# Kernel tuning notes

Measured on AMD Instinct MI355X. Metric: run time of the kernel, lower is better.

Reference implementation:

```python
import jax, jax.numpy as jnp
import numpy as np

B, S, D, H = 2, 2048, 1024, 16
HEAD_DIM = D // H  # 64


def setup_inputs() -> dict:
    key = jax.random.key(0)
    ks = jax.random.split(key, 7)
    x = jax.random.normal(ks[0], (B, S, D), dtype=jnp.float32)
    W_q = jax.random.normal(ks[1], (D, D), dtype=jnp.float32) * 0.02
    W_k = jax.random.normal(ks[2], (D, D), dtype=jnp.float32) * 0.02
    W_v = jax.random.normal(ks[3], (D, D), dtype=jnp.float32) * 0.02
    W_o = jax.random.normal(ks[4], (D, D), dtype=jnp.float32) * 0.02 / np.sqrt(2 * 12)
    b_o = jnp.zeros((D,), dtype=jnp.float32)
    # Ragged prefix attention_mask: per-row valid lengths in [S/2, S];
    # row 0 forced to full length so max_valid_len == S statically (jit-safe).
    lengths = jax.random.randint(ks[5], (B,), S // 2, S + 1)
    lengths = lengths.at[0].set(S)
    attention_mask = (jnp.arange(S)[None, :] < lengths[:, None]).astype(jnp.float32)
    return {"x": x, "attention_mask": attention_mask, "W_q": W_q, "W_k": W_k,
            "W_v": W_v, "W_o": W_o, "b_o": b_o}


def reference(x, attention_mask, W_q, W_k, W_v, W_o, b_o):
    b, s, d = x.shape
    h, hd = H, HEAD_DIM
    # QKV projections (no bias, qkv_bias=False)
    q = (x @ W_q.T).reshape(b, s, h, hd).transpose(0, 2, 1, 3)  # [b,h,s,hd]
    # Masking keys/values at invalid (padded) positions; for prefix masks this
    # is exactly the module's per-batch packing loop (max_valid_len == s).
    m = attention_mask[:, None, :, None]  # [b,1,s,1]
    k = ((x @ W_k.T).reshape(b, s, h, hd).transpose(0, 2, 1, 3)) * m
    v = ((x @ W_v.T).reshape(b, s, h, hd).transpose(0, 2, 1, 3)) * m
    # Naive causal attention, same op order as the torch module:
    # mask with -inf first, then scale by 1/sqrt(head_dim), then softmax.
    causal = jnp.triu(jnp.ones((s, s), dtype=bool), 1)  # True above diagonal
    scores = jnp.einsum('bhqd,bhkd->bhqk', q, k)
    scores = jnp.where(causal[None, None], -jnp.inf, scores)
    att = jax.nn.softmax(scores / jnp.sqrt(jnp.float32(hd)), axis=-1)
    ctx = jnp.einsum('bhqk,bhkd->bhqd', att, v)  # [b,h,s,hd]
    ctx = ctx.transpose(0, 2, 1, 3).reshape(b, s, d)
    # Output projection (dropout is inference no-op)
    return ctx @ W_o.T + b_o
```

## Files before the change

### kernel.cpp

```cpp
#include <hip/hip_runtime.h>

#define B_  2
#define S_  2048
#define D_  1024
#define H_  16
#define HD_ 64
#define N3_ 3072
#define M_  4096

typedef _Float16 f16;
typedef _Float16 f16x2 __attribute__((ext_vector_type(2)));
typedef _Float16 f16x4 __attribute__((ext_vector_type(4)));
typedef _Float16 f16x8 __attribute__((ext_vector_type(8)));
typedef float    f32x4 __attribute__((ext_vector_type(4)));

__device__ __forceinline__ void async16(const f16* g, f16* l) {
  __builtin_amdgcn_global_load_lds(
      (const __attribute__((address_space(1))) unsigned int*)g,
      (__attribute__((address_space(3))) unsigned int*)l, 16, 0, 0);
}

__device__ __forceinline__ f16x2 pkrtz(float a, float b) {
  return __builtin_bit_cast(f16x2, __builtin_amdgcn_cvt_pkrtz(a, b));
}

__global__ __launch_bounds__(256)
void cvt_all(const float* __restrict__ x,
             const float* __restrict__ Wq, const float* __restrict__ Wk,
             const float* __restrict__ Wv, const float* __restrict__ Wo,
             f16* __restrict__ xb, f16* __restrict__ wdst, float qscale) {
  const int i = blockIdx.x * 256 + threadIdx.x;
  const int XN4 = M_ * D_ / 4;
  const int WN4 = D_ * D_ / 4;
  const float* src;
  f16* dst;
  float scale = 1.0f;
  int j;
  if (i < XN4) {
    src = x; dst = xb; j = i;
  } else {
    int k = i - XN4;
    int m = k >> 18;
    j = k & (WN4 - 1);
    src = (m == 0) ? Wq : (m == 1) ? Wk : (m == 2) ? Wv : Wo;
    if (m == 0) scale = qscale;
    dst = wdst + (size_t)m * D_ * D_;
  }
  float4 v = ((const float4*)src)[j];
  f16x4 o = { (f16)(v.x * scale), (f16)(v.y * scale),
              (f16)(v.z * scale), (f16)(v.w * scale) };
  ((f16x4*)dst)[j] = o;
}

__global__ __launch_bounds__(256)
void gemm_qkv(const f16* __restrict__ A, const f16* __restrict__ Bw,
              f16* __restrict__ Cq, f16* __restrict__ vtout,
              const float* __restrict__ mask) {
  __shared__ f16 As[128 * 64];
  __shared__ f16 Bs[128 * 64];

  const int tid  = threadIdx.x;
  const int lane = tid & 63;
  const int w    = tid >> 6;
  const int lcol = lane & 15;
  const int quad = lane >> 4;
  const int lx   = lcol & 7;
  const int wave_m = w >> 1, wave_n = w & 1;

  const int m0 = blockIdx.y * 128;
  const int n0 = blockIdx.x * 128;

  const int rr  = lane >> 3;
  const int gch = (lane & 7) ^ rr;

  const f16* gA[4];
  const f16* gB[4];
  f16* lA[4];
  f16* lB[4];
#pragma unroll
  for (int i = 0; i < 4; i++) {
    int seg = i * 4 + w;
    int row = seg * 8 + rr;
    gA[i] = A  + (size_t)(m0 + row) * D_ + gch * 8;
    gB[i] = Bw + (size_t)(n0 + row) * D_ + gch * 8;
    lA[i] = As + seg * 512;
    lB[i] = Bs + seg * 512;
  }

  int offA[4], offB[4];
#pragma unroll
  for (int i = 0; i < 4; i++) {
    offA[i] = (wave_m * 64 + i * 16 + lcol) * 64;
    offB[i] = (wave_n * 64 + i * 16 + lcol) * 64;
  }

  const f32x4 zero = {0.f, 0.f, 0.f, 0.f};
  f32x4 acc[4][4];
#pragma unroll
  for (int i = 0; i < 4; i++)
#pragma unroll
    for (int j = 0; j < 4; j++) acc[i][j] = zero;

  for (int k0 = 0; k0 < D_; k0 += 64) {
    __syncthreads();
#pragma unroll
    for (int i = 0; i < 4; i++) async16(gA[i] + k0, lA[i]);
#pragma unroll
    for (int i = 0; i < 4; i++) async16(gB[i] + k0, lB[i]);
    __syncthreads();

#pragma unroll
    for (int ks = 0; ks < 2; ks++) {
      const int co = ((quad + 4 * ks) ^ lx) * 8;
      f16x8 af[4], bf[4];
#pragma unroll
      for (int i = 0; i < 4; i++) af[i] = *(const f16x8*)(As + offA[i] + co);
#pragma unroll
      for (int i = 0; i < 4; i++) bf[i] = *(const f16x8*)(Bs + offB[i] + co);
#pragma unroll
      for (int mi = 0; mi < 4; mi++)
#pragma unroll
        for (int ni = 0; ni < 4; ni++)
          acc[mi][ni] = __builtin_amdgcn_mfma_f32_16x16x32_f16(
              af[mi], bf[ni], acc[mi][ni], 0, 0, 0);
    }
  }

  if (n0 >= 2 * D_) {
#pragma unroll
    for (int mi = 0; mi < 4; mi++) {
      const int mgb = m0 + wave_m * 64 + mi * 16 + quad * 4;
      const int b = mgb >> 11, s = mgb & (S_ - 1);
      const float mk0 = mask[mgb], mk1 = mask[mgb + 1];
      const float mk2 = mask[mgb + 2], mk3 = mask[mgb + 3];
#pragma unroll
      for (int ni = 0; ni < 4; ni++) {
        const int vcol = n0 - 2 * D_ + wave_n * 64 + ni * 16 + lcol;
        f16x4 v = { (f16)(acc[mi][ni][0] * mk0), (f16)(acc[mi][ni][1] * mk1),
                    (f16)(acc[mi][ni][2] * mk2), (f16)(acc[mi][ni][3] * mk3) };
        *(f16x4*)(vtout +
                  ((size_t)(b * 16 + (vcol >> 6)) * 64 + (vcol & 63)) * S_ + s) = v;
      }
    }
  } else {
    const bool kmask = (n0 >= D_);
#pragma unroll
    for (int mi = 0; mi < 4; mi++) {
#pragma unroll
      for (int r = 0; r < 4; r++) {
        int mg = m0 + wave_m * 64 + mi * 16 + quad * 4 + r;
        float mk = kmask ? mask[mg] : 1.0f;
#pragma unroll
        for (int ni = 0; ni < 4; ni++) {
          int ng = n0 + wave_n * 64 + ni * 16 + lcol;
          Cq[(size_t)mg * N3_ + ng] = (f16)(acc[mi][ni][r] * mk);
        }
      }
    }
  }
}

__global__ __launch_bounds__(256)
void gemm_proj(const f16* __restrict__ A, const f16* __restrict__ Bw,
               float* __restrict__ Cf, const float* __restrict__ bias) {
  __shared__ f16 As[64 * 64];
  __shared__ f16 Bs[128 * 64];

  const int tid  = threadIdx.x;
  const int lane = tid & 63;
  const int w    = tid >> 6;
  const int lcol = lane & 15;
  const int quad = lane >> 4;
  const int lx   = lcol & 7;
  const int wave_m = w >> 1, wave_n = w & 1;

  const int m0 = blockIdx.y * 64;
  const int n0 = blockIdx.x * 128;

  const int rr  = lane >> 3;
  const int gch = (lane & 7) ^ rr;

  const f16* gA[2];
  const f16* gB[4];
  f16* lA[2];
  f16* lB[4];
#pragma unroll
  for (int i = 0; i < 2; i++) {
    int seg = 2 * w + i;
    gA[i] = A + (size_t)(m0 + seg * 8 + rr) * D_ + gch * 8;
    lA[i] = As + seg * 512;
  }
#pragma unroll
  for (int i = 0; i < 4; i++) {
    int seg = i * 4 + w;
    gB[i] = Bw + (size_t)(n0 + seg * 8 + rr) * D_ + gch * 8;
    lB[i] = Bs + seg * 512;
  }

  int offA[2], offB[4];
#pragma unroll
  for (int i = 0; i < 2; i++) offA[i] = (wave_m * 32 + i * 16 + lcol) * 64;
#pragma unroll
  for (int i = 0; i < 4; i++) offB[i] = (wave_n * 64 + i * 16 + lcol) * 64;

  const f32x4 zero = {0.f, 0.f, 0.f, 0.f};
  f32x4 acc[2][4];
#pragma unroll
  for (int i = 0; i < 2; i++)
#pragma unroll
    for (int j = 0; j < 4; j++) acc[i][j] = zero;

  for (int k0 = 0; k0 < D_; k0 += 64) {
    __syncthreads();
#pragma unroll
    for (int i = 0; i < 2; i++) async16(gA[i] + k0, lA[i]);
#pragma unroll
    for (int i = 0; i < 4; i++) async16(gB[i] + k0, lB[i]);
    __syncthreads();

#pragma unroll
    for (int ks = 0; ks < 2; ks++) {
      const int co = ((quad + 4 * ks) ^ lx) * 8;
      f16x8 af[2], bf[4];
#pragma unroll
      for (int i = 0; i < 2; i++) af[i] = *(const f16x8*)(As + offA[i] + co);
#pragma unroll
      for (int i = 0; i < 4; i++) bf[i] = *(const f16x8*)(Bs + offB[i] + co);
#pragma unroll
      for (int mi = 0; mi < 2; mi++)
#pragma unroll
        for (int ni = 0; ni < 4; ni++)
          acc[mi][ni] = __builtin_amdgcn_mfma_f32_16x16x32_f16(
              af[mi], bf[ni], acc[mi][ni], 0, 0, 0);
    }
  }

#pragma unroll
  for (int mi = 0; mi < 2; mi++) {
#pragma unroll
    for (int r = 0; r < 4; r++) {
      int mg = m0 + wave_m * 32 + mi * 16 + quad * 4 + r;
#pragma unroll
      for (int ni = 0; ni < 4; ni++) {
        int ng = n0 + wave_n * 64 + ni * 16 + lcol;
        Cf[(size_t)mg * D_ + ng] = acc[mi][ni][r] + bias[ng];
      }
    }
  }
}

__global__ __launch_bounds__(256)
void flash_attn4(const f16* __restrict__ qkv, const f16* __restrict__ vt,
                 f16* __restrict__ ctx) {
  __shared__ f16 Ks[64 * 64];
  __shared__ f16 Vs[64 * 64];

  const int tid  = threadIdx.x;
  const int lane = tid & 63;
  const int w    = tid >> 6;
  const int lcol = lane & 15;
  const int quad = lane >> 4;
  const int lx   = lcol & 7;

  const int id   = blockIdx.x;
  const int bh   = (id & 7) + 8 * ((id >> 3) & 3);
  const int pair = id >> 5;
  const int b    = bh >> 4, h = bh & 15;
  const int qtA  = 31 - pair;
  const int qtB  = pair;

  const int rsub = lane >> 3;
  const int gch  = (lane & 7) ^ rsub;
  const int krow0 = w * 8 + rsub;
  const int krow1 = 32 + w * 8 + rsub;
  const f16* Kg = qkv + (size_t)b * S_ * N3_ + D_ + h * HD_;
  const f16* Vg = vt + (size_t)bh * HD_ * S_;
  f16* ldsK0 = Ks + (w * 8) * 64;
  f16* ldsK1 = Ks + (32 + w * 8) * 64;
  f16* ldsV0 = Vs + (w * 8) * 64;
  f16* ldsV1 = Vs + (32 + w * 8) * 64;

  const f32x4 zero = {0.f, 0.f, 0.f, 0.f};

  const int qrowA = qtA * 64 + w * 16 + lcol;
  const int qrowB = qtB * 64 + w * 16 + lcol;
  const f16* QpA = qkv + (size_t)(b * S_ + qrowA) * N3_ + h * HD_;
  const f16* QpB = qkv + (size_t)(b * S_ + qrowB) * N3_ + h * HD_;
  const f16x8 qbA0 = *(const f16x8*)(QpA + quad * 8);
  const f16x8 qbA1 = *(const f16x8*)(QpA + 32 + quad * 8);
  const f16x8 qbB0 = *(const f16x8*)(QpB + quad * 8);
  const f16x8 qbB1 = *(const f16x8*)(QpB + 32 + quad * 8);

  f32x4 oA[4], oB[4];
  float lpA = 0.f, lpB = 0.f;
#pragma unroll
  for (int i = 0; i < 4; i++) { oA[i] = zero; oB[i] = zero; }

  auto mask_diag = [&](f32x4* sc) {
#pragma unroll
    for (int ct = 0; ct < 4; ct++) {
      int koff = ct * 16 + quad * 4;
      int qoff = w * 16 + lcol;
#pragma unroll
      for (int r = 0; r < 4; r++)
        if (koff + r > qoff) sc[ct][r] = -1e30f;
    }
  };
  auto softmax_tiles = [&](f32x4* sc, f16x4* pf, float& lp) {
#pragma unroll
    for (int ct = 0; ct < 4; ct++) {
      float e0 = exp2f(sc[ct][0]);
      float e1 = exp2f(sc[ct][1]);
      float e2 = exp2f(sc[ct][2]);
      float e3 = exp2f(sc[ct][3]);
      lp += (e0 + e1) + (e2 + e3);
      f16x2 lo = pkrtz(e0, e1);
      f16x2 hi = pkrtz(e2, e3);
      f16x4 p = { lo[0], lo[1], hi[0], hi[1] };
      pf[ct] = p;
    }
  };

  for (int kt = 0; kt <= qtA; kt++) {
    const int kbase = kt * 64;
    __syncthreads();
    async16(Kg + (size_t)(kbase + krow0) * N3_ + gch * 8, ldsK0);
    async16(Kg + (size_t)(kbase + krow1) * N3_ + gch * 8, ldsK1);
    async16(Vg + (size_t)krow0 * S_ + kbase + gch * 8, ldsV0);
    async16(Vg + (size_t)krow1 * S_ + kbase + gch * 8, ldsV1);
    __syncthreads();

    const bool doB = (kt <= qtB);

    f16x8 kf0[4], kf1[4];
    f32x4 scA[4], scB[4];
#pragma unroll
    for (int ct = 0; ct < 4; ct++) {
      const f16* kr = Ks + (ct * 16 + lcol) * 64;
      kf0[ct] = *(const f16x8*)(kr + ((quad    ) ^ lx) * 8);
      kf1[ct] = *(const f16x8*)(kr + ((quad + 4) ^ lx) * 8);
      f32x4 z = zero;
      z = __builtin_amdgcn_mfma_f32_16x16x32_f16(kf0[ct], qbA0, z, 0, 0, 0);
      z = __builtin_amdgcn_mfma_f32_16x16x32_f16(kf1[ct], qbA1, z, 0, 0, 0);
      scA[ct] = z;
    }
    if (doB) {
#pragma unroll
      for (int ct = 0; ct < 4; ct++) {
        f32x4 z = zero;
        z = __builtin_amdgcn_mfma_f32_16x16x32_f16(kf0[ct], qbB0, z, 0, 0, 0);
        z = __builtin_amdgcn_mfma_f32_16x16x32_f16(kf1[ct], qbB1, z, 0, 0, 0);
        scB[ct] = z;
      }
    }

    if (kt == qtA) mask_diag(scA);
    if (doB && kt == qtB) mask_diag(scB);

    f16x4 pfA[4], pfB[4];
    softmax_tiles(scA, pfA, lpA);
    if (doB) softmax_tiles(scB, pfB, lpB);

#pragma unroll
    for (int ht = 0; ht < 4; ht++) {
      const f16* vr = Vs + (ht * 16 + lcol) * 64 + (quad & 1) * 4;
      f16x4 vf[4];
#pragma unroll
      for (int ct = 0; ct < 4; ct++)
        vf[ct] = *(const f16x4*)(vr + (((2 * ct + (quad >> 1)) ^ lx) * 8));
#pragma unroll
      for (int ct = 0; ct < 4; ct++)
        oA[ht] = __builtin_amdgcn_mfma_f32_16x16x16f16(vf[ct], pfA[ct], oA[ht], 0, 0, 0);
      if (doB) {
#pragma unroll
        for (int ct = 0; ct < 4; ct++)
          oB[ht] = __builtin_amdgcn_mfma_f32_16x16x16f16(vf[ct], pfB[ct], oB[ht], 0, 0, 0);
      }
    }
  }

  lpA += __shfl_xor(lpA, 16);
  lpA += __shfl_xor(lpA, 32);
  lpB += __shfl_xor(lpB, 16);
  lpB += __shfl_xor(lpB, 32);
  const float invA = 1.f / lpA;
  const float invB = 1.f / lpB;
  f16* cpA = ctx + (size_t)(b * S_ + qrowA) * D_ + h * HD_ + quad * 4;
  f16* cpB = ctx + (size_t)(b * S_ + qrowB) * D_ + h * HD_ + quad * 4;
#pragma unroll
  for (int ht = 0; ht < 4; ht++) {
    f16x4 ovA = { (f16)(oA[ht][0] * invA), (f16)(oA[ht][1] * invA),
                  (f16)(oA[ht][2] * invA), (f16)(oA[ht][3] * invA) };
    *(f16x4*)(cpA + ht * 16) = ovA;
    f16x4 ovB = { (f16)(oB[ht][0] * invB), (f16)(oB[ht][1] * invB),
                  (f16)(oB[ht][2] * invB), (f16)(oB[ht][3] * invB) };
    *(f16x4*)(cpB + ht * 16) = ovB;
  }
}

extern "C" void kernel_launch(void* const* d_in, const int* in_sizes, int n_in,
                              void* d_out, int out_size, void* d_ws, size_t ws_size,
                              hipStream_t stream) {
  (void)in_sizes; (void)n_in; (void)out_size; (void)ws_size;
  const float* x  = (const float*)d_in[0];
  const float* am = (const float*)d_in[1];
  const float* Wq = (const float*)d_in[2];
  const float* Wk = (const float*)d_in[3];
  const float* Wv = (const float*)d_in[4];
  const float* Wo = (const float*)d_in[5];
  const float* bo = (const float*)d_in[6];
  float* out = (float*)d_out;

  f16* ws   = (f16*)d_ws;
  f16* wqkv = ws;
  f16* wo16 = wqkv + (size_t)3 * D_ * D_;
  f16* xb   = wo16 + (size_t)D_ * D_;
  f16* qkvb = xb + (size_t)M_ * D_;
  f16* vtb  = qkvb + (size_t)M_ * N3_;
  f16* ctxb = vtb + (size_t)M_ * D_;

  const float qscale = 0.125f * 1.4426950408889634f;

  cvt_all<<<dim3((M_ * D_ + 4 * D_ * D_) / 1024), 256, 0, stream>>>(
      x, Wq, Wk, Wv, Wo, xb, wqkv, qscale);

  gemm_qkv<<<dim3(N3_ / 128, M_ / 128), 256, 0, stream>>>(
      xb, wqkv, qkvb, vtb, am);
  flash_attn4<<<dim3(512), 256, 0, stream>>>(qkvb, vtb, ctxb);
  gemm_proj<<<dim3(D_ / 128, M_ / 64), 256, 0, stream>>>(
      ctxb, wo16, out, bo);
}
```

Measured before the change: 187.3 us.

## Split attention into one query tile per block and shrink projection tile

```diff
diff --git a/kernel.cpp b/kernel.cpp
--- a/kernel.cpp
+++ b/kernel.cpp
@@ -164,7 +164,7 @@
 void gemm_proj(const f16* __restrict__ A, const f16* __restrict__ Bw,
                float* __restrict__ Cf, const float* __restrict__ bias) {
   __shared__ f16 As[64 * 64];
-  __shared__ f16 Bs[128 * 64];
+  __shared__ f16 Bs[64 * 64];
 
   const int tid  = threadIdx.x;
   const int lane = tid & 63;
@@ -175,61 +175,58 @@
   const int wave_m = w >> 1, wave_n = w & 1;
 
   const int m0 = blockIdx.y * 64;
-  const int n0 = blockIdx.x * 128;
+  const int n0 = blockIdx.x * 64;
 
   const int rr  = lane >> 3;
   const int gch = (lane & 7) ^ rr;
 
   const f16* gA[2];
-  const f16* gB[4];
+  const f16* gB[2];
   f16* lA[2];
-  f16* lB[4];
+  f16* lB[2];
 #pragma unroll
   for (int i = 0; i < 2; i++) {
     int seg = 2 * w + i;
-    gA[i] = A + (size_t)(m0 + seg * 8 + rr) * D_ + gch * 8;
+    gA[i] = A  + (size_t)(m0 + seg * 8 + rr) * D_ + gch * 8;
+    gB[i] = Bw + (size_t)(n0 + seg * 8 + rr) * D_ + gch * 8;
     lA[i] = As + seg * 512;
-  }
-#pragma unroll
-  for (int i = 0; i < 4; i++) {
-    int seg = i * 4 + w;
-    gB[i] = Bw + (size_t)(n0 + seg * 8 + rr) * D_ + gch * 8;
     lB[i] = Bs + seg * 512;
   }
 
-  int offA[2], offB[4];
-#pragma unroll
-  for (int i = 0; i < 2; i++) offA[i] = (wave_m * 32 + i * 16 + lcol) * 64;
-#pragma unroll
-  for (int i = 0; i < 4; i++) offB[i] = (wave_n * 64 + i * 16 + lcol) * 64;
+  int offA[2], offB[2];
+#pragma unroll
+  for (int i = 0; i < 2; i++) {
+    offA[i] = (wave_m * 32 + i * 16 + lcol) * 64;
+    offB[i] = (wave_n * 32 + i * 16 + lcol) * 64;
+  }
 
   const f32x4 zero = {0.f, 0.f, 0.f, 0.f};
-  f32x4 acc[2][4];
+  f32x4 acc[2][2];
 #pragma unroll
   for (int i = 0; i < 2; i++)
 #pragma unroll
-    for (int j = 0; j < 4; j++) acc[i][j] = zero;
+    for (int j = 0; j < 2; j++) acc[i][j] = zero;
 
   for (int k0 = 0; k0 < D_; k0 += 64) {
     __syncthreads();
 #pragma unroll
     for (int i = 0; i < 2; i++) async16(gA[i] + k0, lA[i]);
 #pragma unroll
-    for (int i = 0; i < 4; i++) async16(gB[i] + k0, lB[i]);
+    for (int i = 0; i < 2; i++) async16(gB[i] + k0, lB[i]);
     __syncthreads();
 
 #pragma unroll
     for (int ks = 0; ks < 2; ks++) {
       const int co = ((quad + 4 * ks) ^ lx) * 8;
-      f16x8 af[2], bf[4];
+      f16x8 af[2], bf[2];
 #pragma unroll
       for (int i = 0; i < 2; i++) af[i] = *(const f16x8*)(As + offA[i] + co);
 #pragma unroll
-      for (int i = 0; i < 4; i++) bf[i] = *(const f16x8*)(Bs + offB[i] + co);
+      for (int i = 0; i < 2; i++) bf[i] = *(const f16x8*)(Bs + offB[i] + co);
 #pragma unroll
       for (int mi = 0; mi < 2; mi++)
 #pragma unroll
-        for (int ni = 0; ni < 4; ni++)
+        for (int ni = 0; ni < 2; ni++)
           acc[mi][ni] = __builtin_amdgcn_mfma_f32_16x16x32_f16(
               af[mi], bf[ni], acc[mi][ni], 0, 0, 0);
     }
@@ -241,8 +238,8 @@
     for (int r = 0; r < 4; r++) {
       int mg = m0 + wave_m * 32 + mi * 16 + quad * 4 + r;
 #pragma unroll
-      for (int ni = 0; ni < 4; ni++) {
-        int ng = n0 + wave_n * 64 + ni * 16 + lcol;
+      for (int ni = 0; ni < 2; ni++) {
+        int ng = n0 + wave_n * 32 + ni * 16 + lcol;
         Cf[(size_t)mg * D_ + ng] = acc[mi][ni][r] + bias[ng];
       }
     }
@@ -250,7 +247,7 @@
 }
 
 __global__ __launch_bounds__(256)
-void flash_attn4(const f16* __restrict__ qkv, const f16* __restrict__ vt,
+void flash_attn8(const f16* __restrict__ qkv, const f16* __restrict__ vt,
                  f16* __restrict__ ctx) {
   __shared__ f16 Ks[64 * 64];
   __shared__ f16 Vs[64 * 64];
@@ -264,10 +261,8 @@
 
   const int id   = blockIdx.x;
   const int bh   = (id & 7) + 8 * ((id >> 3) & 3);
-  const int pair = id >> 5;
+  const int qt   = 31 - (id >> 5);
   const int b    = bh >> 4, h = bh & 15;
-  const int qtA  = 31 - pair;
-  const int qtB  = pair;
 
   const int rsub = lane >> 3;
   const int gch  = (lane & 7) ^ rsub;
@@ -282,31 +277,47 @@
 
   const f32x4 zero = {0.f, 0.f, 0.f, 0.f};
 
-  const int qrowA = qtA * 64 + w * 16 + lcol;
-  const int qrowB = qtB * 64 + w * 16 + lcol;
-  const f16* QpA = qkv + (size_t)(b * S_ + qrowA) * N3_ + h * HD_;
-  const f16* QpB = qkv + (size_t)(b * S_ + qrowB) * N3_ + h * HD_;
-  const f16x8 qbA0 = *(const f16x8*)(QpA + quad * 8);
-  const f16x8 qbA1 = *(const f16x8*)(QpA + 32 + quad * 8);
-  const f16x8 qbB0 = *(const f16x8*)(QpB + quad * 8);
-  const f16x8 qbB1 = *(const f16x8*)(QpB + 32 + quad * 8);
-
-  f32x4 oA[4], oB[4];
-  float lpA = 0.f, lpB = 0.f;
-#pragma unroll
-  for (int i = 0; i < 4; i++) { oA[i] = zero; oB[i] = zero; }
-
-  auto mask_diag = [&](f32x4* sc) {
+  const int qrow = qt * 64 + w * 16 + lcol;
+  const f16* Qp = qkv + (size_t)(b * S_ + qrow) * N3_ + h * HD_;
+  const f16x8 qb0 = *(const f16x8*)(Qp + quad * 8);
+  const f16x8 qb1 = *(const f16x8*)(Qp + 32 + quad * 8);
+
+  f32x4 o[4];
+  float lp = 0.f;
+#pragma unroll
+  for (int i = 0; i < 4; i++) o[i] = zero;
+
+  for (int kt = 0; kt <= qt; kt++) {
+    const int kbase = kt * 64;
+    __syncthreads();
+    async16(Kg + (size_t)(kbase + krow0) * N3_ + gch * 8, ldsK0);
+    async16(Kg + (size_t)(kbase + krow1) * N3_ + gch * 8, ldsK1);
+    async16(Vg + (size_t)krow0 * S_ + kbase + gch * 8, ldsV0);
+    async16(Vg + (size_t)krow1 * S_ + kbase + gch * 8, ldsV1);
+    __syncthreads();
+
+    f32x4 sc[4];
 #pragma unroll
     for (int ct = 0; ct < 4; ct++) {
-      int koff = ct * 16 + quad * 4;
-      int qoff = w * 16 + lcol;
-#pragma unroll
-      for (int r = 0; r < 4; r++)
-        if (koff + r > qoff) sc[ct][r] = -1e30f;
-    }
-  };
-  auto softmax_tiles = [&](f32x4* sc, f16x4* pf, float& lp) {
+      const f16* kr = Ks + (ct * 16 + lcol) * 64;
+      f16x8 k0 = *(const f16x8*)(kr + ((quad    ) ^ lx) * 8);
+      f16x8 k1 = *(const f16x8*)(kr + ((quad + 4) ^ lx) * 8);
+      f32x4 z = zero;
+      z = __builtin_amdgcn_mfma_f32_16x16x32_f16(k0, qb0, z, 0, 0, 0);
+      z = __builtin_amdgcn_mfma_f32_16x16x32_f16(k1, qb1, z, 0, 0, 0);
+      sc[ct] = z;
+    }
+    if (kt == qt) {
+#pragma unroll
+      for (int ct = 0; ct < 4; ct++) {
+        int koff = ct * 16 + quad * 4;
+        int qoff = w * 16 + lcol;
+#pragma unroll
+        for (int r = 0; r < 4; r++)
+          if (koff + r > qoff) sc[ct][r] = -1e30f;
+      }
+    }
+    f16x4 pf[4];
 #pragma unroll
     for (int ct = 0; ct < 4; ct++) {
       float e0 = exp2f(sc[ct][0]);
@@ -319,48 +330,6 @@
       f16x4 p = { lo[0], lo[1], hi[0], hi[1] };
       pf[ct] = p;
     }
-  };
-
-  for (int kt = 0; kt <= qtA; kt++) {
-    const int kbase = kt * 64;
-    __syncthreads();
-    async16(Kg + (size_t)(kbase + krow0) * N3_ + gch * 8, ldsK0);
-    async16(Kg + (size_t)(kbase + krow1) * N3_ + gch * 8, ldsK1);
-    async16(Vg + (size_t)krow0 * S_ + kbase + gch * 8, ldsV0);
-    async16(Vg + (size_t)krow1 * S_ + kbase + gch * 8, ldsV1);
-    __syncthreads();
-
-    const bool doB = (kt <= qtB);
-
-    f16x8 kf0[4], kf1[4];
-    f32x4 scA[4], scB[4];
-#pragma unroll
-    for (int ct = 0; ct < 4; ct++) {
-      const f16* kr = Ks + (ct * 16 + lcol) * 64;
-      kf0[ct] = *(const f16x8*)(kr + ((quad    ) ^ lx) * 8);
-      kf1[ct] = *(const f16x8*)(kr + ((quad + 4) ^ lx) * 8);
-      f32x4 z = zero;
-      z = __builtin_amdgcn_mfma_f32_16x16x32_f16(kf0[ct], qbA0, z, 0, 0, 0);
-      z = __builtin_amdgcn_mfma_f32_16x16x32_f16(kf1[ct], qbA1, z, 0, 0, 0);
-      scA[ct] = z;
-    }
-    if (doB) {
-#pragma unroll
-      for (int ct = 0; ct < 4; ct++) {
-        f32x4 z = zero;
-        z = __builtin_amdgcn_mfma_f32_16x16x32_f16(kf0[ct], qbB0, z, 0, 0, 0);
-        z = __builtin_amdgcn_mfma_f32_16x16x32_f16(kf1[ct], qbB1, z, 0, 0, 0);
-        scB[ct] = z;
-      }
-    }
-
-    if (kt == qtA) mask_diag(scA);
-    if (doB && kt == qtB) mask_diag(scB);
-
-    f16x4 pfA[4], pfB[4];
-    softmax_tiles(scA, pfA, lpA);
-    if (doB) softmax_tiles(scB, pfB, lpB);
-
 #pragma unroll
     for (int ht = 0; ht < 4; ht++) {
       const f16* vr = Vs + (ht * 16 + lcol) * 64 + (quad & 1) * 4;
@@ -370,31 +339,19 @@
         vf[ct] = *(const f16x4*)(vr + (((2 * ct + (quad >> 1)) ^ lx) * 8));
 #pragma unroll
       for (int ct = 0; ct < 4; ct++)
-        oA[ht] = __builtin_amdgcn_mfma_f32_16x16x16f16(vf[ct], pfA[ct], oA[ht], 0, 0, 0);
-      if (doB) {
-#pragma unroll
-        for (int ct = 0; ct < 4; ct++)
-          oB[ht] = __builtin_amdgcn_mfma_f32_16x16x16f16(vf[ct], pfB[ct], oB[ht], 0, 0, 0);
-      }
-    }
-  }
-
-  lpA += __shfl_xor(lpA, 16);
-  lpA += __shfl_xor(lpA, 32);
-  lpB += __shfl_xor(lpB, 16);
-  lpB += __shfl_xor(lpB, 32);
-  const float invA = 1.f / lpA;
-  const float invB = 1.f / lpB;
-  f16* cpA = ctx + (size_t)(b * S_ + qrowA) * D_ + h * HD_ + quad * 4;
-  f16* cpB = ctx + (size_t)(b * S_ + qrowB) * D_ + h * HD_ + quad * 4;
+        o[ht] = __builtin_amdgcn_mfma_f32_16x16x16f16(vf[ct], pf[ct], o[ht], 0, 0, 0);
+    }
+  }
+
+  lp += __shfl_xor(lp, 16);
+  lp += __shfl_xor(lp, 32);
+  const float inv = 1.f / lp;
+  f16* cp = ctx + (size_t)(b * S_ + qrow) * D_ + h * HD_ + quad * 4;
 #pragma unroll
   for (int ht = 0; ht < 4; ht++) {
-    f16x4 ovA = { (f16)(oA[ht][0] * invA), (f16)(oA[ht][1] * invA),
-                  (f16)(oA[ht][2] * invA), (f16)(oA[ht][3] * invA) };
-    *(f16x4*)(cpA + ht * 16) = ovA;
-    f16x4 ovB = { (f16)(oB[ht][0] * invB), (f16)(oB[ht][1] * invB),
-                  (f16)(oB[ht][2] * invB), (f16)(oB[ht][3] * invB) };
-    *(f16x4*)(cpB + ht * 16) = ovB;
+    f16x4 ov = { (f16)(o[ht][0] * inv), (f16)(o[ht][1] * inv),
+                 (f16)(o[ht][2] * inv), (f16)(o[ht][3] * inv) };
+    *(f16x4*)(cp + ht * 16) = ov;
   }
 }
 
@@ -426,7 +383,7 @@
 
   gemm_qkv<<<dim3(N3_ / 128, M_ / 128), 256, 0, stream>>>(
       xb, wqkv, qkvb, vtb, am);
-  flash_attn4<<<dim3(512), 256, 0, stream>>>(qkvb, vtb, ctxb);
-  gemm_proj<<<dim3(D_ / 128, M_ / 64), 256, 0, stream>>>(
+  flash_attn8<<<dim3(1024), 256, 0, stream>>>(qkvb, vtb, ctxb);
+  gemm_proj<<<dim3(D_ / 64, M_ / 64), 256, 0, stream>>>(
       ctxb, wo16, out, bo);
 }
```

Measured after the change: 188.0 us. Within noise of the previous version (+0.4%).
